# Optimization experiments

Hardware: AMD Instinct MI355X
Metric: run time of the kernel (lower is better)

Reference implementation:

```python
import jax, jax.numpy as jnp
import numpy as np

B, T_E, T_D, H = 32, 128, 128, 256  # batch, encoder len, decoder len, hidden


def lstm_scan(x, h0, c0, Wih, Whh, bih, bhh):
    """Single-layer PyTorch-style LSTM over x: [B, T, F] -> (hs, cs) each [T, B, H]."""
    bias = bih + bhh

    def step(carry, xt):
        h, c = carry
        gates = xt @ Wih.T + h @ Whh.T + bias  # [B, 4H], gate order i,f,g,o
        i, f, g, o = jnp.split(gates, 4, axis=-1)
        i = jax.nn.sigmoid(i)
        f = jax.nn.sigmoid(f)
        o = jax.nn.sigmoid(o)
        g = jnp.tanh(g)
        c = f * c + i * g
        h = o * jnp.tanh(c)
        return (h, c), (h, c)

    _, (hs, cs) = jax.lax.scan(step, (h0, c0), jnp.swapaxes(x, 0, 1))
    return hs, cs


def setup_inputs() -> dict:
    key = jax.random.key(0)
    ks = jax.random.split(key, 16)
    seq = jax.random.normal(ks[0], (B, T_E), jnp.float32)
    seq_m = jax.random.randint(ks[1], (B, 1), 1, T_E + 1)  # valid lengths in [1, T_E]
    pos = jnp.arange(T_E)[None, :]
    seq = jnp.where(pos < seq_m, seq, 0.0)  # zero-pad beyond length (drives the mask)
    target = jax.random.normal(ks[2], (B, T_D), jnp.float32)

    s = 0.1
    nrm = lambda k, shape: s * jax.random.normal(k, shape, jnp.float32)
    return dict(
        seq=seq, seq_m=seq_m, target=target,
        Wih_e=nrm(ks[3], (4 * H, 1)), Whh_e=nrm(ks[4], (4 * H, H)),
        bih_e=nrm(ks[5], (4 * H,)), bhh_e=nrm(ks[6], (4 * H,)),
        Wih_d=nrm(ks[7], (4 * H, 1)), Whh_d=nrm(ks[8], (4 * H, H)),
        bih_d=nrm(ks[9], (4 * H,)), bhh_d=nrm(ks[10], (4 * H,)),
        We=nrm(ks[11], (H, H)), be=nrm(ks[12], (H,)),
        Wd=nrm(ks[13], (H, H)), bd=nrm(ks[14], (H,)),
        v=jnp.ones((H,), jnp.float32),
    )


def reference(seq, seq_m, target,
              Wih_e, Whh_e, bih_e, bhh_e,
              Wih_d, Whh_d, bih_d, bhh_d,
              We, be, Wd, bd, v):
    zeros = jnp.zeros((B, H), seq.dtype)
    # Encoder: one fused scan instead of the original per-timestep Python loop
    hs_e, cs_e = lstm_scan(seq[..., None], zeros, zeros, Wih_e, Whh_e, bih_e, bhh_e)
    e = jnp.swapaxes(hs_e, 0, 1)  # [B, T_E, H]

    # Grab encoder state at the last valid step (seq_m - 1) per batch element
    last = seq_m[:, 0] - 1  # [B]
    bidx = jnp.arange(B)
    e_hs = hs_e[last, bidx]  # [B, H]
    e_cs = cs_e[last, bidx]

    # Decoder initialized from the selected encoder state
    hs_d, _ = lstm_scan(target[..., None], e_hs, e_cs, Wih_d, Whh_d, bih_d, bhh_d)
    d = jnp.swapaxes(hs_d, 0, 1)  # [B, T_D, H]

    e2 = e @ We.T + be  # [B, T_E, H]
    d2 = d @ Wd.T + bd  # [B, T_D, H]

    # Additive (Bahdanau) attention: tanh(e_j + d_i) . v  -> [B, T_D, T_E]
    t = jnp.tanh(d2[:, :, None, :] + e2[:, None, :, :])  # [B, T_D, T_E, H]
    p = jnp.einsum('bijh,h->bij', t, v)

    # Masking: original sets seq[:,0]=0.1 then adds 1000 where seq value nonzero,
    # after subtracting 1000 everywhere -> padded (zero) positions end up at -1000.
    seq0 = seq.at[:, 0].set(0.1)
    mask = (seq0 != 0).astype(p.dtype)  # [B, T_E]
    p = p + (mask[:, None, :] - 1.0) * 1000.0

    return jax.nn.softmax(p, axis=-1)  # pointer distribution over encoder positions
```

## Files before the change

kernel.cpp:

```cpp
#include <hip/hip_runtime.h>
#include <hip/hip_bf16.h>

#define BB 32
#define TT 128
#define HH 256
#define G4 4
#define UPB 64
#define RPB 256

#define AGENT __HIP_MEMORY_SCOPE_AGENT
#define AL(p) __hip_atomic_load((p), __ATOMIC_RELAXED, AGENT)

__device__ __forceinline__ float rcp_f(float x) { return __builtin_amdgcn_rcpf(x); }
__device__ __forceinline__ float sigmoid_f(float x) {
    return rcp_f(1.f + __expf(-x));
}
__device__ __forceinline__ float tanh_f(float x) {
    float e = __expf(2.f * x);
    return 1.f - 2.f * rcp_f(e + 1.f);
}

__device__ __forceinline__ void bar_lds() {
    asm volatile("s_waitcnt lgkmcnt(0)\n\ts_barrier" ::: "memory");
}

__global__ __launch_bounds__(512, 2) void lstm_kernel(
    const float* __restrict__ seq,
    const int* __restrict__ seq_m,
    const float* __restrict__ target,
    const float* __restrict__ Wih_e,
    const float* __restrict__ Whh_e,
    const float* __restrict__ bih_e, const float* __restrict__ bhh_e,
    const float* __restrict__ Wih_d, const float* __restrict__ Whh_d,
    const float* __restrict__ bih_d, const float* __restrict__ bhh_d,
    const float* __restrict__ We, const float* __restrict__ be,
    const float* __restrict__ Wd, const float* __restrict__ bd,
    float* __restrict__ e2,
    float* __restrict__ d2,
    unsigned long long* __restrict__ mbox,
    unsigned long long* __restrict__ hsave)
{
    const int blk = blockIdx.x;
    const int b = blk & 31;
    const int g = blk >> 5;
    const int tid = threadIdx.x;
    const int row_local = tid >> 1;
    const int half = tid & 1;
    const int gate = row_local >> 6;
    const int u_local = row_local & 63;
    const int row_global = gate * HH + g * UPB + u_local;
    const int last = seq_m[b] - 1;
    const int s = tid - 256;
    const int pu = s >> 2;
    const int kq = s & 3;
    const int pcol = g * UPB + pu;

    __shared__ float hbuf[2][HH];
    __shared__ float g_lds[RPB];
    __shared__ float x_lds[2 * TT];
    __shared__ float h_final[HH];

    for (int i = tid; i < TT; i += 512) {
        x_lds[i] = seq[b * TT + i];
        x_lds[TT + i] = target[b * TT + i];
    }

    float4 w[32];
    float bias_r, wih_r;
    auto loadw = [&](const float* Whh, const float* Wih,
                     const float* bih, const float* bhh) {
        const float4* wr = (const float4*)(Whh + row_global * HH + half * 128);
#pragma unroll
        for (int i = 0; i < 32; ++i) w[i] = wr[i];
        bias_r = bih[row_global] + bhh[row_global];
        wih_r = Wih[row_global];
    };
    loadw(Whh_e, Wih_e, bih_e, bhh_e);

    float4 pw[16];
    float pb = 0.f;
    auto loadp = [&](const float* W, const float* bias) {
        const float4* src = (const float4*)(W + pcol * HH + kq * 64);
#pragma unroll
        for (int i = 0; i < 16; ++i) pw[i] = src[i];
        pb = bias[pcol];
    };
    if (tid >= 256) loadp(We, be);

    auto projdot = [&](const float* hsrc) -> float {
        const float4* hp = (const float4*)(hsrc + kq * 64);
        float pa = 0.f;
#pragma unroll
        for (int i = 0; i < 16; ++i) {
            float4 hv = hp[i];
            pa = fmaf(pw[i].x, hv.x, pa);
            pa = fmaf(pw[i].y, hv.y, pa);
            pa = fmaf(pw[i].z, hv.z, pa);
            pa = fmaf(pw[i].w, hv.w, pa);
        }
        pa += __shfl_xor(pa, 1);
        pa += __shfl_xor(pa, 2);
        return pa + pb;
    };

    if (tid < 64) {
        ((float4*)hbuf[1])[tid] = make_float4(0.f, 0.f, 0.f, 0.f);
    }
    __syncthreads();

    float c = 0.f, c_saved = 0.f, h_saved = 0.f;

    for (int t = 0; t < 2 * TT; ++t) {
        const int phase = t >> 7;
        const int tt = t & 127;
        const float x = x_lds[t];
        const int rb = (t & 1) ^ 1;

        const float4* h4 = ((const float4*)hbuf[rb]) + half * 32;
        float4 a4 = make_float4(0.f, 0.f, 0.f, 0.f);
#pragma unroll
        for (int i = 0; i < 32; ++i) {
            float4 hv = h4[i];
            a4.x = fmaf(w[i].x, hv.x, a4.x);
            a4.y = fmaf(w[i].y, hv.y, a4.y);
            a4.z = fmaf(w[i].z, hv.z, a4.z);
            a4.w = fmaf(w[i].w, hv.w, a4.w);
        }
        float acc = (a4.x + a4.y) + (a4.z + a4.w);
        acc += __shfl_xor(acc, 1);
        float gv = acc + bias_r + x * wih_r;
        if (half == 0) g_lds[row_local] = gv;
        bar_lds();

        if (tid < 64) {
            float gi = g_lds[tid];
            float gf = g_lds[64 + tid];
            float gg = g_lds[128 + tid];
            float go = g_lds[192 + tid];
            float si = sigmoid_f(gi);
            float sf = sigmoid_f(gf);
            float tg = tanh_f(gg);
            float so = sigmoid_f(go);
            c = sf * c + si * tg;
            float h = so * tanh_f(c);
            const int ug = g * UPB + tid;
            unsigned long long pkt =
                ((unsigned long long)(unsigned)(t + 1) << 32) | __float_as_uint(h);
            __hip_atomic_store(&mbox[(t & 1) * BB * HH + b * HH + ug], pkt,
                               __ATOMIC_RELAXED, AGENT);
            if (phase == 0 && tt == last) {
                c_saved = c;
                h_saved = h;
                unsigned long long spkt =
                    (1ull << 32) | (unsigned long long)__float_as_uint(h);
                __hip_atomic_store(&hsave[b * HH + ug], spkt, __ATOMIC_RELAXED, AGENT);
            }
            hbuf[t & 1][ug] = (t == TT - 1) ? h_saved : h;
        }

        if (tid >= 64 && tid < 256) {
            const int p = (g + (tid >> 6)) & 3;
            const int lane = tid & 63;
            const int ppu = p * UPB + lane;
            unsigned long long* src;
            unsigned want;
            if (t == TT - 1) {
                src = &hsave[b * HH + ppu];
                want = 1u;
            } else {
                src = &mbox[(t & 1) * BB * HH + b * HH + ppu];
                want = (unsigned)(t + 1);
            }
            unsigned long long pv;
            {
                unsigned long long r0 = AL(src);
                unsigned long long r1 = AL(src);
                unsigned long long r2 = AL(src);
                unsigned long long r3 = AL(src);
                for (;;) {
                    if ((unsigned)(r0 >> 32) == want) { pv = r0; break; }
                    r0 = AL(src);
                    if ((unsigned)(r1 >> 32) == want) { pv = r1; break; }
                    r1 = AL(src);
                    if ((unsigned)(r2 >> 32) == want) { pv = r2; break; }
                    r2 = AL(src);
                    if ((unsigned)(r3 >> 32) == want) { pv = r3; break; }
                    r3 = AL(src);
                }
            }
            hbuf[t & 1][ppu] = __uint_as_float((unsigned)pv);
        }

        if (tid >= 256 && t >= 1) {
            const float* hsrc = (t == TT) ? h_final : hbuf[rb];
            float pv = projdot(hsrc);
            if (kq == 0) {
                if (t <= TT)
                    e2[(b * TT + (t - 1)) * HH + pcol] = pv;
                else
                    d2[(b * TT + (t - 1 - TT)) * HH + pcol] = pv;
            }
        }
        if (tid >= 256 && t == TT - 1) {
            unsigned long long* src = &mbox[((TT - 1) & 1) * BB * HH + b * HH + s];
            const unsigned want = (unsigned)TT;
            unsigned long long r0 = AL(src);
            unsigned long long r1 = AL(src);
            unsigned long long pv;
            for (;;) {
                if ((unsigned)(r0 >> 32) == want) { pv = r0; break; }
                r0 = AL(src);
                if ((unsigned)(r1 >> 32) == want) { pv = r1; break; }
                r1 = AL(src);
            }
            h_final[s] = __uint_as_float((unsigned)pv);
        }
        if (tid >= 256 && t == TT) loadp(Wd, bd);

        bar_lds();

        if (t == TT - 1) {
            loadw(Whh_d, Wih_d, bih_d, bhh_d);
            c = c_saved;
        }
    }

    if (tid >= 256) {
        unsigned long long* src = &mbox[((2 * TT - 1) & 1) * BB * HH + b * HH + s];
        const unsigned want = (unsigned)(2 * TT);
        unsigned long long r0 = AL(src);
        unsigned long long r1 = AL(src);
        unsigned long long pv;
        for (;;) {
            if ((unsigned)(r0 >> 32) == want) { pv = r0; break; }
            r0 = AL(src);
            if ((unsigned)(r1 >> 32) == want) { pv = r1; break; }
            r1 = AL(src);
        }
        h_final[s] = __uint_as_float((unsigned)pv);
    }
    __syncthreads();
    if (tid >= 256) {
        float pv = projdot(h_final);
        if (kq == 0) d2[(b * TT + (TT - 1)) * HH + pcol] = pv;
    }
}

#define EPAD 260
__global__ __launch_bounds__(256) void attn_p_kernel(
    const float* __restrict__ e2, const float* __restrict__ d2,
    const float* __restrict__ vv, float* __restrict__ p_ws) {
    __shared__ float e2c[32][EPAD];
    __shared__ float d2t[32][EPAD];
    __shared__ float v_lds[HH];

    const int blk = blockIdx.x;
    const int b = blk >> 4;
    const int i0 = ((blk >> 2) & 3) * 32;
    const int j0 = (blk & 3) * 32;
    const int tid = threadIdx.x;
    const int jl = tid & 31, ig = tid >> 5;

    if (tid < 64) *(float4*)&v_lds[tid * 4] = ((const float4*)vv)[tid];
    for (int idx = tid; idx < 32 * 64; idx += 256) {
        int r = idx >> 6, q = idx & 63;
        *(float4*)&d2t[r][q * 4] = ((const float4*)(d2 + (b * TT + i0 + r) * HH))[q];
        *(float4*)&e2c[r][q * 4] = ((const float4*)(e2 + (b * TT + j0 + r) * HH))[q];
    }
    __syncthreads();

    float a0 = 0.f, a1 = 0.f, a2 = 0.f, a3 = 0.f;
    for (int h = 0; h < HH; h += 4) {
        float4 ev = *(const float4*)&e2c[jl][h];
        float4 vx = *(const float4*)&v_lds[h];
        float4 d0 = *(const float4*)&d2t[ig * 4 + 0][h];
        float4 d1 = *(const float4*)&d2t[ig * 4 + 1][h];
        float4 d2v = *(const float4*)&d2t[ig * 4 + 2][h];
        float4 d3 = *(const float4*)&d2t[ig * 4 + 3][h];
        a0 = fmaf(tanh_f(ev.x + d0.x), vx.x, a0);
        a0 = fmaf(tanh_f(ev.y + d0.y), vx.y, a0);
        a0 = fmaf(tanh_f(ev.z + d0.z), vx.z, a0);
        a0 = fmaf(tanh_f(ev.w + d0.w), vx.w, a0);
        a1 = fmaf(tanh_f(ev.x + d1.x), vx.x, a1);
        a1 = fmaf(tanh_f(ev.y + d1.y), vx.y, a1);
        a1 = fmaf(tanh_f(ev.z + d1.z), vx.z, a1);
        a1 = fmaf(tanh_f(ev.w + d1.w), vx.w, a1);
        a2 = fmaf(tanh_f(ev.x + d2v.x), vx.x, a2);
        a2 = fmaf(tanh_f(ev.y + d2v.y), vx.y, a2);
        a2 = fmaf(tanh_f(ev.z + d2v.z), vx.z, a2);
        a2 = fmaf(tanh_f(ev.w + d2v.w), vx.w, a2);
        a3 = fmaf(tanh_f(ev.x + d3.x), vx.x, a3);
        a3 = fmaf(tanh_f(ev.y + d3.y), vx.y, a3);
        a3 = fmaf(tanh_f(ev.z + d3.z), vx.z, a3);
        a3 = fmaf(tanh_f(ev.w + d3.w), vx.w, a3);
    }
    float* pr = p_ws + (b * TT + i0 + ig * 4) * TT + j0 + jl;
    pr[0 * TT] = a0;
    pr[1 * TT] = a1;
    pr[2 * TT] = a2;
    pr[3 * TT] = a3;
}

__global__ __launch_bounds__(256) void attn_sm_kernel(
    const float* __restrict__ p_ws, const float* __restrict__ seq,
    float* __restrict__ out) {
    const int blk = blockIdx.x;
    const int b = blk >> 3;
    const int r0 = (blk & 7) * 16;
    const int tid = threadIdx.x;
    const int r = tid >> 4, l16 = tid & 15;
    const int row = (b * TT + r0 + r) * TT;

    float xr[8];
    float m = -1e30f;
#pragma unroll
    for (int k = 0; k < 8; ++k) {
        const int j = l16 + 16 * k;
        float x = p_ws[row + j];
        float sv = (j == 0) ? 0.1f : seq[b * TT + j];
        if (sv == 0.f) x -= 1000.f;
        xr[k] = x;
        m = fmaxf(m, x);
    }
#pragma unroll
    for (int o = 8; o >= 1; o >>= 1) m = fmaxf(m, __shfl_xor(m, o));
    float s = 0.f;
#pragma unroll
    for (int k = 0; k < 8; ++k) {
        xr[k] = __expf(xr[k] - m);
        s += xr[k];
    }
#pragma unroll
    for (int o = 8; o >= 1; o >>= 1) s += __shfl_xor(s, o);
    float inv = rcp_f(s);
#pragma unroll
    for (int k = 0; k < 8; ++k) out[row + l16 + 16 * k] = xr[k] * inv;
}

extern "C" void kernel_launch(void* const* d_in, const int* in_sizes, int n_in,
                              void* d_out, int out_size, void* d_ws, size_t ws_size,
                              hipStream_t stream) {
    const float* seq = (const float*)d_in[0];
    const int* seq_m = (const int*)d_in[1];
    const float* target = (const float*)d_in[2];
    const float* Wih_e = (const float*)d_in[3];
    const float* Whh_e = (const float*)d_in[4];
    const float* bih_e = (const float*)d_in[5];
    const float* bhh_e = (const float*)d_in[6];
    const float* Wih_d = (const float*)d_in[7];
    const float* Whh_d = (const float*)d_in[8];
    const float* bih_d = (const float*)d_in[9];
    const float* bhh_d = (const float*)d_in[10];
    const float* We = (const float*)d_in[11];
    const float* be = (const float*)d_in[12];
    const float* Wd = (const float*)d_in[13];
    const float* bd = (const float*)d_in[14];
    const float* vv = (const float*)d_in[15];

    float* ws = (float*)d_ws;
    const size_t SZ_ED = (size_t)BB * TT * HH;
    float* e2 = ws;
    float* d2 = e2 + SZ_ED;
    float* p_ws = d2 + SZ_ED;
    unsigned long long* mbox =
        (unsigned long long*)(p_ws + (size_t)BB * TT * TT);
    unsigned long long* hsave = mbox + 2 * BB * HH;

    const size_t needed = (2 * SZ_ED + (size_t)BB * TT * TT) * sizeof(float) +
                          3 * BB * HH * sizeof(unsigned long long);
    if (ws_size < needed) return;

    hipMemsetAsync(mbox, 0, 3 * BB * HH * sizeof(unsigned long long), stream);
    lstm_kernel<<<BB * G4, 512, 0, stream>>>(seq, seq_m, target, Wih_e, Whh_e, bih_e,
                                             bhh_e, Wih_d, Whh_d, bih_d, bhh_d, We,
                                             be, Wd, bd, e2, d2, mbox, hsave);
    attn_p_kernel<<<512, 256, 0, stream>>>(e2, d2, vv, p_ws);
    attn_sm_kernel<<<256, 256, 0, stream>>>(p_ws, seq, (float*)d_out);
}
```

Baseline: 659.6 us.

## Map gate rows to adjacent lanes and combine gates with shuffles instead of LDS barrier

Thread-to-row mapping changes so that the four gate rows for one hidden unit (two halves each) sit in eight adjacent lanes. The gate values are then exchanged with warp shuffles rather than written to shared memory and read back after a block barrier. This removes one LDS round-trip and one barrier per timestep on the serial recurrence path. The elementwise gate math now runs on one lane in eight across all waves instead of on a single wave, and the polling threads are remapped to tid<192 with a shifted peer index.

```diff
diff --git a/kernel.cpp b/kernel.cpp
--- a/kernel.cpp
+++ b/kernel.cpp
@@ -6,7 +6,6 @@
 #define HH 256
 #define G4 4
 #define UPB 64
-#define RPB 256
 
 #define AGENT __HIP_MEMORY_SCOPE_AGENT
 #define AL(p) __hip_atomic_load((p), __ATOMIC_RELAXED, AGENT)
@@ -44,11 +43,12 @@
     const int b = blk & 31;
     const int g = blk >> 5;
     const int tid = threadIdx.x;
-    const int row_local = tid >> 1;
-    const int half = tid & 1;
-    const int gate = row_local >> 6;
-    const int u_local = row_local & 63;
-    const int row_global = gate * HH + g * UPB + u_local;
+    const int u = tid >> 3;
+    const int j8 = tid & 7;
+    const int gate = j8 >> 1;
+    const int half = j8 & 1;
+    const int row_global = gate * HH + g * UPB + u;
+    const int ug = g * UPB + u;
     const int last = seq_m[b] - 1;
     const int s = tid - 256;
     const int pu = s >> 2;
@@ -56,7 +56,6 @@
     const int pcol = g * UPB + pu;
 
     __shared__ float hbuf[2][HH];
-    __shared__ float g_lds[RPB];
     __shared__ float x_lds[2 * TT];
     __shared__ float h_final[HH];
 
@@ -129,21 +128,17 @@
         float acc = (a4.x + a4.y) + (a4.z + a4.w);
         acc += __shfl_xor(acc, 1);
         float gv = acc + bias_r + x * wih_r;
-        if (half == 0) g_lds[row_local] = gv;
-        bar_lds();
-
-        if (tid < 64) {
-            float gi = g_lds[tid];
-            float gf = g_lds[64 + tid];
-            float gg = g_lds[128 + tid];
-            float go = g_lds[192 + tid];
-            float si = sigmoid_f(gi);
-            float sf = sigmoid_f(gf);
-            float tg = tanh_f(gg);
-            float so = sigmoid_f(go);
+        float x2v = __shfl_xor(gv, 2);
+        float x4v = __shfl_xor(gv, 4);
+        float x6v = __shfl_xor(x2v, 4);
+
+        if (j8 == 0) {
+            float si = sigmoid_f(gv);
+            float sf = sigmoid_f(x2v);
+            float tg = tanh_f(x4v);
+            float so = sigmoid_f(x6v);
             c = sf * c + si * tg;
             float h = so * tanh_f(c);
-            const int ug = g * UPB + tid;
             unsigned long long pkt =
                 ((unsigned long long)(unsigned)(t + 1) << 32) | __float_as_uint(h);
             __hip_atomic_store(&mbox[(t & 1) * BB * HH + b * HH + ug], pkt,
@@ -158,8 +153,8 @@
             hbuf[t & 1][ug] = (t == TT - 1) ? h_saved : h;
         }
 
-        if (tid >= 64 && tid < 256) {
-            const int p = (g + (tid >> 6)) & 3;
+        if (tid < 192) {
+            const int p = (g + 1 + (tid >> 6)) & 3;
             const int lane = tid & 63;
             const int ppu = p * UPB + lane;
             unsigned long long* src;
```

Result: slower. 818.7 us (+24.1%).
